# Performance work log

Hardware: AMD Instinct MI355X
Metric: run time of the kernel (lower is better)

## Reference

```python
import jax, jax.numpy as jnp
import numpy as np

SR_CUT = 10.0
N_ATOMS = 10000
N_PAIRS = 250000
K = 128          # radial basis size
H = 128          # interaction / output hidden width
NB = 5           # num_blocks
NIL = 2          # num_interaction_layers
NOL = 2          # num_output_layers
NO = 2           # num_outputs


def setup_inputs() -> dict:
    key = jax.random.key(0)
    ks = jax.random.split(key, 10)
    Z = jax.random.randint(ks[0], (N_ATOMS,), 0, 95)
    R = jax.random.normal(ks[1], (N_ATOMS, 3), dtype=jnp.float32) * 3.0
    idx_i = jnp.sort(jax.random.randint(ks[2], (N_PAIRS,), 0, N_ATOMS))
    idx_j = jax.random.randint(ks[3], (N_PAIRS,), 0, N_ATOMS)
    s = 0.05
    iW = jax.random.normal(ks[4], (NB, NIL, H, H), dtype=jnp.float32) * s
    iB = jnp.zeros((NB, NIL, H), dtype=jnp.float32)
    oW = jax.random.normal(ks[5], (NB, NOL, H, H), dtype=jnp.float32) * s
    oB = jnp.zeros((NB, NOL, H), dtype=jnp.float32)
    oWf = jax.random.normal(ks[6], (NB, H, NO), dtype=jnp.float32) * s
    oBf = jnp.zeros((NB, NO), dtype=jnp.float32)
    scales = jnp.ones((NO, 95), dtype=jnp.float32)
    shifts = jnp.zeros((NO, 95), dtype=jnp.float32)
    return {"Z": Z, "R": R, "idx_i": idx_i, "idx_j": idx_j,
            "iW": iW, "iB": iB, "oW": oW, "oB": oB,
            "oWf": oWf, "oBf": oBf, "scales": scales, "shifts": shifts}


def _ssp(x):
    # shifted softplus: softplus(x) - log(2)
    return jax.nn.softplus(x) - jnp.log(2.0).astype(x.dtype)


def _basis(rij):
    # smooth polynomial cutoff + Gaussian basis on exp(-r) (PhysNet-style 'Default' radial basis)
    x = rij / SR_CUT
    fcut = jnp.where(rij < SR_CUT, 1.0 - 6.0 * x**5 + 15.0 * x**4 - 10.0 * x**3, 0.0)
    mu = jnp.linspace(np.exp(-SR_CUT), 1.0, K, dtype=rij.dtype)          # [K]
    width = ((2.0 / K) * (1.0 - np.exp(-SR_CUT))) ** (-2)
    er = jnp.exp(-rij)[:, None]                                          # [P,1]
    return fcut[:, None] * jnp.exp(-width * (er - mu) ** 2)              # [P,K]


def reference(Z, R, idx_i, idx_j, iW, iB, oW, oB, oWf, oBf, scales, shifts):
    # pairwise distances via gather (bf_layer.getPairs)
    D = R[idx_j] - R[idx_i]                                              # [P,3]
    rij = jnp.sqrt(jnp.sum(D * D, axis=-1) + 1e-12)                      # [P]
    bf = _basis(rij)                                                     # [P,K]

    x = bf
    outputs = jnp.zeros((N_ATOMS, NO), dtype=R.dtype)
    nhloss = jnp.zeros((), dtype=R.dtype)
    lastout2 = None
    for b in range(NB):
        # interaction block: per-edge MLP (K==H so stacked weights are uniform)
        for l in range(NIL):
            x = _ssp(x @ iW[b, l] + iB[b, l])
        # output block: per-edge MLP + final linear head
        y = x
        for l in range(NOL):
            y = _ssp(y @ oW[b, l] + oB[b, l])
        out_e = y @ oWf[b] + oBf[b]                                      # [P,NO]
        out = jax.ops.segment_sum(out_e, idx_i, num_segments=N_ATOMS)    # [N,NO]
        outputs = outputs + out
        out2 = out ** 2
        if b > 0:
            nhloss = nhloss + jnp.mean(out2 / (out2 + lastout2 + 1e-7))
        lastout2 = out2

    sc = scales[:, Z].T                                                  # [N,NO]
    sh = shifts[:, Z].T                                                  # [N,NO]
    outputs = outputs * sc + sh
    return outputs, rij, nhloss
```

## Files before the change

kernel.cpp:

```cpp
#include <hip/hip_runtime.h>
#include <stdint.h>

#define NP   250000
#define NA   10000
#define NBLK 5
#define NL   20
#define BLOB_W_BYTES 16384
#define BLOB_BYTES   16896

#define LOG2E 1.4426950408889634f
#define LN2   0.6931471805599453f

typedef float  f32x4  __attribute__((ext_vector_type(4)));
typedef unsigned short ushort_t;
typedef unsigned int   uint_t;
typedef int4  i4_ma __attribute__((may_alias));
typedef uint2 u2_ma __attribute__((may_alias));
typedef uint_t u1_ma __attribute__((may_alias));

#if __has_builtin(__builtin_amdgcn_exp2f)
#define FEXP2(x) __builtin_amdgcn_exp2f(x)
#else
#define FEXP2(x) exp2f(x)
#endif
#if __has_builtin(__builtin_amdgcn_logf)
#define FLOG2(x) __builtin_amdgcn_logf(x)
#else
#define FLOG2(x) log2f(x)
#endif

__device__ uint8_t g_blob[NL * BLOB_BYTES];
__device__ float   g_outs[NBLK * NA * 2];
__device__ float   g_nh[1];
__device__ unsigned g_done;
__device__ float   g_Rf[NA * 3];
__device__ float   g_oWfF[NBLK * 128 * 2];
__device__ float   g_oBfF[NBLK * 2];
__device__ float   g_scF[190];
__device__ float   g_shF[190];

static __device__ __forceinline__ float bf2f(ushort_t u) {
    return __uint_as_float(((uint_t)u) << 16);
}
static __device__ uint8_t f2fp8(float f) {
    uint_t u = __float_as_uint(f);
    uint8_t s = (uint8_t)((u >> 24) & 0x80);
    float af = fabsf(f);
    if (af != af) return (uint8_t)(s | 0x7F);
    if (af > 448.0f) return (uint8_t)(s | 0x7E);
    int e = (int)((u >> 23) & 0xFF) - 127;
    uint_t m = u & 0x7FFFFFu;
    if (e >= -6) {
        uint_t mant = m >> 20;
        uint_t rest = m & 0xFFFFFu;
        if (rest > 0x80000u || (rest == 0x80000u && (mant & 1u))) mant++;
        uint_t ee = (uint_t)(e + 7);
        if (mant == 8u) { mant = 0u; ee++; }
        if (ee > 15u || (ee == 15u && mant > 6u)) return (uint8_t)(s | 0x7E);
        return (uint8_t)(s | (ee << 3) | mant);
    }
    int qq = (int)rintf(af * 512.0f);
    if (qq > 7) return (uint8_t)(s | 0x08);
    return (uint8_t)(s | (uint_t)qq);
}
template <bool HI>
static __device__ __forceinline__ int cvtpk2(float a, float b, int old) {
#if __has_builtin(__builtin_amdgcn_cvt_pk_fp8_f32)
    return __builtin_amdgcn_cvt_pk_fp8_f32(a, b, old, HI);
#else
    int p = (int)f2fp8(a) | ((int)f2fp8(b) << 8);
    return HI ? (int)((old & 0x0000FFFF) | ((uint_t)p << 16))
              : (int)((old & 0xFFFF0000) | (uint_t)p);
#endif
}
static __device__ __forceinline__ long u2l(u2_ma v) {
    union { u2_ma u; long l; } x; x.u = v; return x.l;
}
static __device__ __forceinline__ float ssp_u(float accv) {
    return FLOG2(0.5f + FEXP2(accv));
}

static __device__ __forceinline__ bool detect_is_f32(const ushort_t* probe) {
    __shared__ int flag;
    if (threadIdx.x == 0) flag = 0;
    __syncthreads();
    if (threadIdx.x < 256) {
        float v = fabsf(bf2f(probe[2 * threadIdx.x]));
        if (!(v <= 64.0f)) flag = 1;
    }
    __syncthreads();
    return flag != 0;
}
static __device__ __forceinline__ float in_elt(const void* p, int i, bool isf32) {
    return isf32 ? ((const float*)p)[i] : bf2f(((const ushort_t*)p)[i]);
}

__global__ void prep_kernel(const void* __restrict__ iW, const void* __restrict__ iB,
                            const void* __restrict__ oW, const void* __restrict__ oB,
                            const void* __restrict__ R, const void* __restrict__ oWf,
                            const void* __restrict__ oBf, const void* __restrict__ scales,
                            const void* __restrict__ shifts)
{
    const bool isf32 = detect_is_f32((const ushort_t*)iW);
    if (blockIdx.x < 80) {
        const int L = blockIdx.x >> 2;
        const int qr = blockIdx.x & 3;
        const int b = L >> 2, li = L & 3;
        const void* srcW = (li < 2) ? iW : oW;
        const void* srcB = (li < 2) ? iB : oB;
        const int lyr = (li < 2) ? (b * 2 + li) : (b * 2 + li - 2);
        const int wofs = lyr * 16384;
        const int bofs = lyr * 128;
        uint8_t* blob = g_blob + (size_t)L * BLOB_BYTES;
        uint_t* dw = (uint_t*)blob;
        float*  db = (float*)(blob + BLOB_W_BYTES);
        const float sc = (L == 0) ? LOG2E : 1.0f;
        for (int t = threadIdx.x; t < 1024; t += blockDim.x) {
            int d = qr * 1024 + t;
            int n = d & 127, kg = d >> 7;
            float w0 = sc * in_elt(srcW, wofs + (kg * 4 + 0) * 128 + n, isf32);
            float w1 = sc * in_elt(srcW, wofs + (kg * 4 + 1) * 128 + n, isf32);
            float w2 = sc * in_elt(srcW, wofs + (kg * 4 + 2) * 128 + n, isf32);
            float w3 = sc * in_elt(srcW, wofs + (kg * 4 + 3) * 128 + n, isf32);
            int w = cvtpk2<false>(w0, w1, 0);
            w = cvtpk2<true>(w2, w3, w);
            dw[n * 32 + 2 * ((kg >> 1) ^ (n & 15)) + (kg & 1)] = (uint_t)w;
        }
        if (qr == 0)
            for (int m = threadIdx.x; m < 128; m += blockDim.x)
                db[m] = in_elt(srcB, bofs + m, isf32) * LOG2E - 1.0f;
    } else {
        const int t = (blockIdx.x - 80) * 256 + threadIdx.x;
        if (t < NBLK * NA * 2) g_outs[t] = 0.0f;
        if (t == 0) { g_nh[0] = 0.0f; g_done = 0u; }
        if (t < NA * 3)      g_Rf[t]   = in_elt(R, t, isf32);
        if (t < NBLK * 256)  g_oWfF[t] = LN2 * in_elt(oWf, t, isf32);
        if (t < NBLK * 2)    g_oBfF[t] = in_elt(oBf, t, isf32);
        if (t < 190)         g_scF[t]  = in_elt(scales, t, isf32);
        if (t < 190)         g_shF[t]  = in_elt(shifts, t, isf32);
    }
}

__global__ __launch_bounds__(256, 3)
void pairs_mlp_kernel(const int* __restrict__ idx_i,
                      const int* __restrict__ idx_j,
                      float* __restrict__ out_rij)
{
    __shared__ i4_ma w_lds[1024];
    __shared__ u2_ma act_all[4 * 512];

    const int wave = threadIdx.x >> 6;
    const int lane = threadIdx.x & 63;
    u2_ma* act = act_all + wave * 512;
    const u2_ma* wl2 = (const u2_ma*)w_lds;

    const int pp = lane & 31;
    const int p0 = blockIdx.x * 128 + wave * 32;
    const int p = p0 + pp;
    const bool valid = (p < NP);

    int ai = 0, aj = 0;
    if (valid) { ai = idx_i[p]; aj = idx_j[p]; }
    float xi0 = g_Rf[3 * ai + 0], xi1 = g_Rf[3 * ai + 1], xi2 = g_Rf[3 * ai + 2];
    float xj0 = g_Rf[3 * aj + 0], xj1 = g_Rf[3 * aj + 1], xj2 = g_Rf[3 * aj + 2];
    float dx = xj0 - xi0, dy = xj1 - xi1, dz = xj2 - xi2;
    float rij = sqrtf(dx * dx + dy * dy + dz * dz + 1e-12f);
    if (lane < 32 && valid) out_rij[p] = rij;

    float fcut = 0.0f;
    if (valid && rij < 10.0f) {
        float xc = rij * 0.1f;
        float x3 = xc * xc * xc;
        fcut = 1.0f + x3 * (-10.0f + xc * (15.0f - 6.0f * xc));
    }
    const float mu0 = 4.5399929762484854e-05f;
    const float dmu = (1.0f - mu0) / 127.0f;
    const float wc = (2.0f / 128.0f) * (1.0f - mu0);
    const float NW2 = -(1.0f / (wc * wc)) * LOG2E;
    float er = FEXP2(-rij * LOG2E);

    const int q = lane >> 4;
    const int l15 = lane & 15;
    const int aseg = valid ? ai : -1;

    u2_ma bfrX[2][4];
    {
        float er_n[2], fc_n[2];
        er_n[0] = __shfl(er, l15, 64);      fc_n[0] = __shfl(fcut, l15, 64);
        er_n[1] = __shfl(er, 16 + l15, 64); fc_n[1] = __shfl(fcut, 16 + l15, 64);
#pragma unroll
        for (int nt = 0; nt < 2; ++nt)
#pragma unroll
            for (int kt = 0; kt < 4; ++kt) {
                float v[8];
#pragma unroll
                for (int jj = 0; jj < 8; ++jj) {
                    int g = kt * 32 + q * 8 + jj;
                    float mu = mu0 + (float)g * dmu;
                    float e0 = er_n[nt] - mu;
                    v[jj] = fc_n[nt] * FEXP2(NW2 * e0 * e0);
                }
                int w0 = cvtpk2<false>(v[0], v[1], 0);
                w0 = cvtpk2<true>(v[2], v[3], w0);
                int w1 = cvtpk2<false>(v[4], v[5], 0);
                w1 = cvtpk2<true>(v[6], v[7], w1);
                bfrX[nt][kt].x = (uint_t)w0;
                bfrX[nt][kt].y = (uint_t)w1;
            }
    }

    for (int blk = 0; blk < NBLK; ++blk) {
#pragma unroll
        for (int li = 0; li < 4; ++li) {
            const int L = blk * 4 + li;
            const i4_ma* gW = (const i4_ma*)(g_blob + (size_t)L * BLOB_BYTES);
            const float* bb = (const float*)(g_blob + (size_t)L * BLOB_BYTES + BLOB_W_BYTES);

            __syncthreads();
#pragma unroll
            for (int it = 0; it < 4; ++it)
                w_lds[threadIdx.x + it * 256] = gW[threadIdx.x + it * 256];
            __syncthreads();

            f32x4 acc[2][8];
#pragma unroll
            for (int mt = 0; mt < 8; ++mt) {
                const f32x4 bias = *(const f32x4*)(bb + mt * 16 + q * 4);
                acc[0][mt] = bias;
                acc[1][mt] = bias;
            }
#pragma unroll
            for (int kt = 0; kt < 4; ++kt) {
                const int cc = kt * 4 + q;
                u2_ma b0, b1;
                if (li == 0) {
                    b0 = bfrX[0][kt];
                    b1 = bfrX[1][kt];
                } else {
                    b0 = act[(l15) * 16 + (cc ^ l15)];
                    b1 = act[(16 + l15) * 16 + (cc ^ l15)];
                    if (li == 2) { bfrX[0][kt] = b0; bfrX[1][kt] = b1; }
                }
                const long lb0 = u2l(b0), lb1 = u2l(b1);
#pragma unroll
                for (int mt = 0; mt < 8; ++mt) {
                    const long la = u2l(wl2[(mt * 16 + l15) * 16 + (cc ^ l15)]);
                    acc[0][mt] = __builtin_amdgcn_mfma_f32_16x16x32_fp8_fp8(
                        la, lb0, acc[0][mt], 0, 0, 0);
                    acc[1][mt] = __builtin_amdgcn_mfma_f32_16x16x32_fp8_fp8(
                        la, lb1, acc[1][mt], 0, 0, 0);
                }
            }

            if (li < 3) {
#pragma unroll
                for (int mt = 0; mt < 8; ++mt) {
                    const int c = mt * 2 + (q >> 1);
#pragma unroll
                    for (int nt = 0; nt < 2; ++nt) {
                        float u0 = ssp_u(acc[nt][mt][0]);
                        float u1 = ssp_u(acc[nt][mt][1]);
                        float u2 = ssp_u(acc[nt][mt][2]);
                        float u3 = ssp_u(acc[nt][mt][3]);
                        int w = cvtpk2<false>(u0, u1, 0);
                        w = cvtpk2<true>(u2, u3, w);
                        const int rp = nt * 16 + l15;
                        ((u1_ma*)&act[rp * 16 + (c ^ (rp & 15))])[q & 1] = (uint_t)w;
                    }
                }
            } else {
                const float* hw = g_oWfF + blk * 256;
                const float ob0 = g_oBfF[blk * 2 + 0];
                const float ob1 = g_oBfF[blk * 2 + 1];
                float hs[2][2];
#pragma unroll
                for (int nt = 0; nt < 2; ++nt) {
                    float h0 = 0.f, h1 = 0.f;
#pragma unroll
                    for (int mt = 0; mt < 8; ++mt) {
#pragma unroll
                        for (int rr = 0; rr < 4; ++rr) {
                            float u = ssp_u(acc[nt][mt][rr]);
                            const int f = mt * 16 + q * 4 + rr;
                            h0 = fmaf(u, hw[f * 2 + 0], h0);
                            h1 = fmaf(u, hw[f * 2 + 1], h1);
                        }
                    }
                    h0 += __shfl_xor(h0, 16, 64);
                    h0 += __shfl_xor(h0, 32, 64);
                    h1 += __shfl_xor(h1, 16, 64);
                    h1 += __shfl_xor(h1, 32, 64);
                    hs[nt][0] = h0; hs[nt][1] = h1;
                }
                float c0v = (pp < 16) ? hs[0][0] : hs[1][0];
                float c1v = (pp < 16) ? hs[0][1] : hs[1][1];
                c0v += ob0; c1v += ob1;
#pragma unroll
                for (int d = 1; d < 32; d <<= 1) {
                    float t0 = __shfl_up(c0v, d, 64);
                    float t1 = __shfl_up(c1v, d, 64);
                    int   an = __shfl_up(aseg, d, 64);
                    if (pp >= d && an == aseg) { c0v += t0; c1v += t1; }
                }
                int ain = __shfl_down(aseg, 1, 64);
                bool tail = (pp == 31) || (ain != aseg);
                if (lane < 32 && valid && tail) {
                    atomicAdd(&g_outs[(blk * NA + aseg) * 2 + 0], c0v);
                    atomicAdd(&g_outs[(blk * NA + aseg) * 2 + 1], c1v);
                }
            }
        }
    }
}

__global__ void finalize_kernel(const int* __restrict__ Z,
                                float* __restrict__ out_atoms,
                                float* __restrict__ out_nh)
{
    __shared__ float red[256];
    const int a = blockIdx.x * 256 + threadIdx.x;
    float s = 0.f;
    if (a < NA) {
        float v[NBLK][2];
        float t0 = 0.f, t1 = 0.f;
#pragma unroll
        for (int b = 0; b < NBLK; ++b) {
            v[b][0] = g_outs[(b * NA + a) * 2 + 0];
            v[b][1] = g_outs[(b * NA + a) * 2 + 1];
            t0 += v[b][0]; t1 += v[b][1];
        }
        const int z = Z[a];
        out_atoms[a * 2 + 0] = t0 * g_scF[z]      + g_shF[z];
        out_atoms[a * 2 + 1] = t1 * g_scF[95 + z] + g_shF[95 + z];
#pragma unroll
        for (int b = 1; b < NBLK; ++b)
#pragma unroll
            for (int o = 0; o < 2; ++o) {
                float x2 = v[b][o] * v[b][o];
                float p2 = v[b - 1][o] * v[b - 1][o];
                s += x2 / (x2 + p2 + 1e-7f);
            }
    }
    red[threadIdx.x] = s;
    __syncthreads();
    for (int st = 128; st > 0; st >>= 1) {
        if (threadIdx.x < st) red[threadIdx.x] += red[threadIdx.x + st];
        __syncthreads();
    }
    if (threadIdx.x == 0) {
        atomicAdd(&g_nh[0], red[0]);
        __threadfence();
        unsigned old = atomicAdd(&g_done, 1u);
        if (old == gridDim.x - 1) {
            float v = atomicAdd(&g_nh[0], 0.0f);
            out_nh[0] = v * (1.0f / 20000.0f);
        }
    }
}

extern "C" void kernel_launch(void* const* d_in, const int* in_sizes, int n_in,
                              void* d_out, int out_size, void* d_ws, size_t ws_size,
                              hipStream_t stream)
{
    const int* Z     = (const int*)d_in[0];
    const void* R    = d_in[1];
    const int* idx_i = (const int*)d_in[2];
    const int* idx_j = (const int*)d_in[3];
    const void* iW   = d_in[4];
    const void* iB   = d_in[5];
    const void* oW   = d_in[6];
    const void* oB   = d_in[7];
    const void* oWf  = d_in[8];
    const void* oBf  = d_in[9];
    const void* scales = d_in[10];
    const void* shifts = d_in[11];

    float* out_f = (float*)d_out;

    prep_kernel<<<80 + 391, 256, 0, stream>>>(iW, iB, oW, oB, R, oWf, oBf, scales, shifts);
    pairs_mlp_kernel<<<(NP + 127) / 128, 256, 0, stream>>>(idx_i, idx_j, out_f + 2 * NA);
    finalize_kernel<<<(NA + 255) / 256, 256, 0, stream>>>(Z, out_f, out_f + 2 * NA + NP);
}
```

Baseline: 268.7 us.

## Double-buffer layer weights in LDS via async global_load_lds prefetch

Measured after the change: 276.0 us. 2.7% more time.

```diff
diff --git a/kernel.cpp b/kernel.cpp
--- a/kernel.cpp
+++ b/kernel.cpp
@@ -17,6 +17,8 @@
 typedef int4  i4_ma __attribute__((may_alias));
 typedef uint2 u2_ma __attribute__((may_alias));
 typedef uint_t u1_ma __attribute__((may_alias));
+
+#define FENCE() asm volatile("" ::: "memory")
 
 #if __has_builtin(__builtin_amdgcn_exp2f)
 #define FEXP2(x) __builtin_amdgcn_exp2f(x)
@@ -78,6 +80,26 @@
 }
 static __device__ __forceinline__ float ssp_u(float accv) {
     return FLOG2(0.5f + FEXP2(accv));
+}
+
+static __device__ __forceinline__ void stage_w(int L, i4_ma* dst) {
+    const uint8_t* gsrc = g_blob + (size_t)L * BLOB_BYTES;
+    const int wave = threadIdx.x >> 6;
+#pragma unroll
+    for (int it = 0; it < 4; ++it) {
+        const uint32_t* gp = (const uint32_t*)(gsrc + (((size_t)(it * 256) + threadIdx.x) << 4));
+        uint32_t* lp = (uint32_t*)&dst[it * 256 + wave * 64];
+        __builtin_amdgcn_global_load_lds(
+            (const __attribute__((address_space(1))) uint32_t*)gp,
+            (__attribute__((address_space(3))) uint32_t*)lp,
+            16, 0, 0);
+    }
+}
+static __device__ __forceinline__ void load_bias(f32x4* bv, int L, int q) {
+    const float* nb = (const float*)(g_blob + (size_t)L * BLOB_BYTES + BLOB_W_BYTES);
+#pragma unroll
+    for (int mt = 0; mt < 8; ++mt)
+        bv[mt] = *(const f32x4*)(nb + mt * 16 + q * 4);
 }
 
 static __device__ __forceinline__ bool detect_is_f32(const ushort_t* probe) {
@@ -146,13 +168,13 @@
                       const int* __restrict__ idx_j,
                       float* __restrict__ out_rij)
 {
-    __shared__ i4_ma w_lds[1024];
+    __shared__ i4_ma w_lds0[1024];
+    __shared__ i4_ma w_lds1[1024];
     __shared__ u2_ma act_all[4 * 512];
 
     const int wave = threadIdx.x >> 6;
     const int lane = threadIdx.x & 63;
     u2_ma* act = act_all + wave * 512;
-    const u2_ma* wl2 = (const u2_ma*)w_lds;
 
     const int pp = lane & 31;
     const int p0 = blockIdx.x * 128 + wave * 32;
@@ -173,15 +195,23 @@
         float x3 = xc * xc * xc;
         fcut = 1.0f + x3 * (-10.0f + xc * (15.0f - 6.0f * xc));
     }
+
+    const int q = lane >> 4;
+    const int l15 = lane & 15;
+    const int aseg = valid ? ai : -1;
+
+    FENCE();
+    stage_w(0, w_lds0);
+    stage_w(1, w_lds1);
+    f32x4 biasv[8];
+    load_bias(biasv, 0, q);
+    FENCE();
+
     const float mu0 = 4.5399929762484854e-05f;
     const float dmu = (1.0f - mu0) / 127.0f;
     const float wc = (2.0f / 128.0f) * (1.0f - mu0);
     const float NW2 = -(1.0f / (wc * wc)) * LOG2E;
     float er = FEXP2(-rij * LOG2E);
-
-    const int q = lane >> 4;
-    const int l15 = lane & 15;
-    const int aseg = valid ? ai : -1;
 
     u2_ma bfrX[2][4];
     {
@@ -213,21 +243,18 @@
 #pragma unroll
         for (int li = 0; li < 4; ++li) {
             const int L = blk * 4 + li;
-            const i4_ma* gW = (const i4_ma*)(g_blob + (size_t)L * BLOB_BYTES);
-            const float* bb = (const float*)(g_blob + (size_t)L * BLOB_BYTES + BLOB_W_BYTES);
-
-            __syncthreads();
-#pragma unroll
-            for (int it = 0; it < 4; ++it)
-                w_lds[threadIdx.x + it * 256] = gW[threadIdx.x + it * 256];
-            __syncthreads();
+            const u2_ma* wl2 = (const u2_ma*)((li & 1) ? w_lds1 : w_lds0);
+            i4_ma* wbuf = (li & 1) ? w_lds1 : w_lds0;
+
+            asm volatile("s_waitcnt vmcnt(4)" ::: "memory");
+            __builtin_amdgcn_s_barrier();
+            FENCE();
 
             f32x4 acc[2][8];
 #pragma unroll
             for (int mt = 0; mt < 8; ++mt) {
-                const f32x4 bias = *(const f32x4*)(bb + mt * 16 + q * 4);
-                acc[0][mt] = bias;
-                acc[1][mt] = bias;
+                acc[0][mt] = biasv[mt];
+                acc[1][mt] = biasv[mt];
             }
 #pragma unroll
             for (int kt = 0; kt < 4; ++kt) {
@@ -308,6 +335,19 @@
                     atomicAdd(&g_outs[(blk * NA + aseg) * 2 + 0], c0v);
                     atomicAdd(&g_outs[(blk * NA + aseg) * 2 + 1], c1v);
                 }
+            }
+
+            {
+                int Lb = L + 1; if (Lb >= NL) Lb = 0;
+                load_bias(biasv, Lb, q);
+                FENCE();
+            }
+            __builtin_amdgcn_s_barrier();
+            FENCE();
+            {
+                int Ls = L + 2; if (Ls >= NL) Ls -= NL;
+                stage_w(Ls, wbuf);
+                FENCE();
             }
         }
     }
```

## Split MFMA output tiles into two passes to cut registers and raise occupancy

Applied to the files above, without the earlier changes.

Result: slower. 283.2 us (+5.4%).

```diff
diff --git a/kernel.cpp b/kernel.cpp
--- a/kernel.cpp
+++ b/kernel.cpp
@@ -141,7 +141,7 @@
     }
 }
 
-__global__ __launch_bounds__(256, 3)
+__global__ __launch_bounds__(256, 4)
 void pairs_mlp_kernel(const int* __restrict__ idx_i,
                       const int* __restrict__ idx_j,
                       float* __restrict__ out_rij)
@@ -222,70 +222,94 @@
                 w_lds[threadIdx.x + it * 256] = gW[threadIdx.x + it * 256];
             __syncthreads();
 
-            f32x4 acc[2][8];
-#pragma unroll
-            for (int mt = 0; mt < 8; ++mt) {
-                const f32x4 bias = *(const f32x4*)(bb + mt * 16 + q * 4);
-                acc[0][mt] = bias;
-                acc[1][mt] = bias;
+            u2_ma bB[2][4];
+            if (li == 0) {
+#pragma unroll
+                for (int kt = 0; kt < 4; ++kt) { bB[0][kt] = bfrX[0][kt]; bB[1][kt] = bfrX[1][kt]; }
+            } else {
+#pragma unroll
+                for (int kt = 0; kt < 4; ++kt) {
+                    const int cc = kt * 4 + q;
+                    bB[0][kt] = act[(l15) * 16 + (cc ^ l15)];
+                    bB[1][kt] = act[(16 + l15) * 16 + (cc ^ l15)];
+                }
+                if (li == 2) {
+#pragma unroll
+                    for (int kt = 0; kt < 4; ++kt) { bfrX[0][kt] = bB[0][kt]; bfrX[1][kt] = bB[1][kt]; }
+                }
             }
-#pragma unroll
-            for (int kt = 0; kt < 4; ++kt) {
-                const int cc = kt * 4 + q;
-                u2_ma b0, b1;
-                if (li == 0) {
-                    b0 = bfrX[0][kt];
-                    b1 = bfrX[1][kt];
+
+            float h0a[2], h1a[2];
+            const float* hw = g_oWfF + blk * 256;
+
+#pragma unroll
+            for (int ps = 0; ps < 2; ++ps) {
+                f32x4 acc[2][4];
+#pragma unroll
+                for (int mtl = 0; mtl < 4; ++mtl) {
+                    const f32x4 bias = *(const f32x4*)(bb + (ps * 4 + mtl) * 16 + q * 4);
+                    acc[0][mtl] = bias;
+                    acc[1][mtl] = bias;
+                }
+#pragma unroll
+                for (int kt = 0; kt < 4; ++kt) {
+                    const int cc = kt * 4 + q;
+                    const long lb0 = u2l(bB[0][kt]), lb1 = u2l(bB[1][kt]);
+#pragma unroll
+                    for (int mtl = 0; mtl < 4; ++mtl) {
+                        const int mt = ps * 4 + mtl;
+                        const long la = u2l(wl2[(mt * 16 + l15) * 16 + (cc ^ l15)]);
+                        acc[0][mtl] = __builtin_amdgcn_mfma_f32_16x16x32_fp8_fp8(
+                            la, lb0, acc[0][mtl], 0, 0, 0);
+                        acc[1][mtl] = __builtin_amdgcn_mfma_f32_16x16x32_fp8_fp8(
+                            la, lb1, acc[1][mtl], 0, 0, 0);
+                    }
+                }
+
+                if (li < 3) {
+#pragma unroll
+                    for (int mtl = 0; mtl < 4; ++mtl) {
+                        const int mt = ps * 4 + mtl;
+                        const int c = mt * 2 + (q >> 1);
+#pragma unroll
+                        for (int nt = 0; nt < 2; ++nt) {
+                            float u0 = ssp_u(acc[nt][mtl][0]);
+                            float u1 = ssp_u(acc[nt][mtl][1]);
+                            float u2 = ssp_u(acc[nt][mtl][2]);
+                            float u3 = ssp_u(acc[nt][mtl][3]);
+                            int w = cvtpk2<false>(u0, u1, 0);
+                            w = cvtpk2<true>(u2, u3, w);
+                            const int rp = nt * 16 + l15;
+                            ((u1_ma*)&act[rp * 16 + (c ^ (rp & 15))])[q & 1] = (uint_t)w;
+                        }
+                    }
                 } else {
-                    b0 = act[(l15) * 16 + (cc ^ l15)];
-                    b1 = act[(16 + l15) * 16 + (cc ^ l15)];
-                    if (li == 2) { bfrX[0][kt] = b0; bfrX[1][kt] = b1; }
-                }
-                const long lb0 = u2l(b0), lb1 = u2l(b1);
-#pragma unroll
-                for (int mt = 0; mt < 8; ++mt) {
-                    const long la = u2l(wl2[(mt * 16 + l15) * 16 + (cc ^ l15)]);
-                    acc[0][mt] = __builtin_amdgcn_mfma_f32_16x16x32_fp8_fp8(
-                        la, lb0, acc[0][mt], 0, 0, 0);
-                    acc[1][mt] = __builtin_amdgcn_mfma_f32_16x16x32_fp8_fp8(
-                        la, lb1, acc[1][mt], 0, 0, 0);
+                    if (ps == 0) { h0a[0] = h0a[1] = 0.f; h1a[0] = h1a[1] = 0.f; }
+#pragma unroll
+                    for (int mtl = 0; mtl < 4; ++mtl) {
+#pragma unroll
+                        for (int rr = 0; rr < 4; ++rr) {
+                            const int f = (ps * 4 + mtl) * 16 + q * 4 + rr;
+                            const float w0 = hw[f * 2 + 0];
+                            const float w1 = hw[f * 2 + 1];
+#pragma unroll
+                            for (int nt = 0; nt < 2; ++nt) {
+                                float u = ssp_u(acc[nt][mtl][rr]);
+                                h0a[nt] = fmaf(u, w0, h0a[nt]);
+                                h1a[nt] = fmaf(u, w1, h1a[nt]);
+                            }
+                        }
+                    }
                 }
             }
 
-            if (li < 3) {
-#pragma unroll
-                for (int mt = 0; mt < 8; ++mt) {
-                    const int c = mt * 2 + (q >> 1);
-#pragma unroll
-                    for (int nt = 0; nt < 2; ++nt) {
-                        float u0 = ssp_u(acc[nt][mt][0]);
-                        float u1 = ssp_u(acc[nt][mt][1]);
-                        float u2 = ssp_u(acc[nt][mt][2]);
-                        float u3 = ssp_u(acc[nt][mt][3]);
-                        int w = cvtpk2<false>(u0, u1, 0);
-                        w = cvtpk2<true>(u2, u3, w);
-                        const int rp = nt * 16 + l15;
-                        ((u1_ma*)&act[rp * 16 + (c ^ (rp & 15))])[q & 1] = (uint_t)w;
-                    }
-                }
-            } else {
-                const float* hw = g_oWfF + blk * 256;
+            if (li == 3) {
                 const float ob0 = g_oBfF[blk * 2 + 0];
                 const float ob1 = g_oBfF[blk * 2 + 1];
                 float hs[2][2];
 #pragma unroll
                 for (int nt = 0; nt < 2; ++nt) {
-                    float h0 = 0.f, h1 = 0.f;
-#pragma unroll
-                    for (int mt = 0; mt < 8; ++mt) {
-#pragma unroll
-                        for (int rr = 0; rr < 4; ++rr) {
-                            float u = ssp_u(acc[nt][mt][rr]);
-                            const int f = mt * 16 + q * 4 + rr;
-                            h0 = fmaf(u, hw[f * 2 + 0], h0);
-                            h1 = fmaf(u, hw[f * 2 + 1], h1);
-                        }
-                    }
+                    float h0 = h0a[nt], h1 = h1a[nt];
                     h0 += __shfl_xor(h0, 16, 64);
                     h0 += __shfl_xor(h0, 32, 64);
                     h1 += __shfl_xor(h1, 16, 64);
```
